# Kernel optimization log

Hardware: AMD Instinct MI355X
Metric: run time of the kernel (lower is better)

Reference implementation:

```python
import jax, jax.numpy as jnp
import numpy as np

B, S, D_IN, D_OUT = 4, 4096, 1024, 1024

def setup_inputs() -> dict:
    key = jax.random.key(0)
    kx, kq, kk, kv = jax.random.split(key, 4)
    # torch Linear weights are [out, in]; init scale ~ U(-1/sqrt(in), 1/sqrt(in))
    lim = 1.0 / np.sqrt(D_IN)
    x = jax.random.normal(kx, (B, S, D_IN), dtype=jnp.float32)
    W_query = jax.random.uniform(kq, (D_OUT, D_IN), dtype=jnp.float32, minval=-lim, maxval=lim)
    W_key = jax.random.uniform(kk, (D_OUT, D_IN), dtype=jnp.float32, minval=-lim, maxval=lim)
    W_value = jax.random.uniform(kv, (D_OUT, D_IN), dtype=jnp.float32, minval=-lim, maxval=lim)
    return {"x": x, "W_query": W_query, "W_key": W_key, "W_value": W_value}

def reference(x, W_query, W_key, W_value):
    # Linear: x @ W.T  (torch convention, weight shape [out, in])
    q = jnp.einsum('bsd,od->bso', x, W_query)
    k = jnp.einsum('bsd,od->bso', x, W_key)
    v = jnp.einsum('bsd,od->bso', x, W_value)
    scale = 1.0 / jnp.sqrt(jnp.asarray(k.shape[-1], dtype=x.dtype))
    scores = jnp.einsum('bqo,bko->bqk', q, k) * scale  # [B,S,S]
    weights = jax.nn.softmax(scores, axis=-1)
    return jnp.einsum('bqk,bko->bqo', weights, v)  # [B,S,D_OUT]
```

## Files before the change

### kernel.cpp

```cpp
#include <hip/hip_runtime.h>
#include <cstdint>
#include <cstddef>

typedef __attribute__((ext_vector_type(8))) short short8;
typedef __attribute__((ext_vector_type(4))) float f32x4;

__device__ __forceinline__ unsigned short f2bf(float x) {
  union { float f; unsigned u; } v; v.f = x;
  unsigned r = (v.u + 0x7FFFu + ((v.u >> 16) & 1u)) >> 16;
  return (unsigned short)r;
}

#define GLOAD16(g, l)                                                    \
  __builtin_amdgcn_global_load_lds(                                      \
      (const __attribute__((address_space(1))) unsigned int*)(g),        \
      (__attribute__((address_space(3))) unsigned int*)(l), 16, 0, 0)

__global__ __launch_bounds__(256) void cvt_f32_bf16(
    const float* __restrict__ in, unsigned short* __restrict__ out, long n) {
  long i = ((long)blockIdx.x * 256 + threadIdx.x) * 8;
  if (i >= n) return;
  const float4* p = (const float4*)(in + i);
  float4 a = p[0], b = p[1];
  short8 r;
  r[0] = (short)f2bf(a.x); r[1] = (short)f2bf(a.y);
  r[2] = (short)f2bf(a.z); r[3] = (short)f2bf(a.w);
  r[4] = (short)f2bf(b.x); r[5] = (short)f2bf(b.y);
  r[6] = (short)f2bf(b.z); r[7] = (short)f2bf(b.w);
  *(short8*)(out + i) = r;
}

template <int MODE>
__global__ __launch_bounds__(512, 2) void gemm_bt256(
    const unsigned short* __restrict__ A, int lda, size_t asb,
    const unsigned short* __restrict__ B, int ldb, size_t bsb,
    void* __restrict__ C, int ldc, size_t csb,
    int nbn, int K, float scale) {
  __shared__ unsigned short As[2][256 * 64];
  __shared__ unsigned short Bs[2][256 * 64];

  A += (size_t)blockIdx.y * asb;
  B += (size_t)blockIdx.y * bsb;
  char* Cb = (char*)C + (size_t)blockIdx.y * csb * (MODE == 3 ? 4 : 2);

  unsigned bid = blockIdx.x;
  unsigned cpx = gridDim.x >> 3;
  unsigned swz = (bid & 7u) * cpx + (bid >> 3);
  int bm = (int)(swz / (unsigned)nbn);
  int bn = (int)(swz % (unsigned)nbn);
  int m0 = bm * 256, n0 = bn * 256;

  int t512 = threadIdx.x;
  int lane = t512 & 63, wid = t512 >> 6;
  int wm = wid >> 2, wn = wid & 3;
  int l15 = lane & 15, l4 = lane >> 4;

  int srow = t512 >> 3;
  int g = (t512 & 7) ^ ((t512 >> 3) & 7);
  const unsigned short* pa = A + (size_t)(m0 + srow) * lda + g * 8;
  const unsigned short* pb = B + (size_t)(n0 + srow) * ldb + g * 8;

  f32x4 acc[8][4] = {};
  f32x4 rsum[8] = {};
  short8 ones;
#pragma unroll
  for (int e = 0; e < 8; e++) ones[e] = (short)0x3F80;

  const int NT = K >> 6;

#define STAGE(jj, buf)                                                    \
  do {                                                                    \
    int _k0 = (jj) << 6;                                                  \
    _Pragma("unroll") for (int i = 0; i < 4; i++)                         \
        GLOAD16(pa + (size_t)(i * 64) * lda + _k0,                        \
                (char*)As[buf] + i * 8192 + t512 * 16);                   \
    _Pragma("unroll") for (int i = 0; i < 4; i++)                         \
        GLOAD16(pb + (size_t)(i * 64) * ldb + _k0,                        \
                (char*)Bs[buf] + i * 8192 + t512 * 16);                   \
  } while (0)

  STAGE(0, 0);

  for (int j = 0; j < NT; ++j) {
    int cur = j & 1;
    __builtin_amdgcn_sched_barrier(0);
    __builtin_amdgcn_s_barrier();
    if (j + 1 < NT) {
      STAGE(j + 1, cur ^ 1);
      asm volatile("s_waitcnt vmcnt(8)" ::: "memory");
    } else {
      asm volatile("s_waitcnt vmcnt(0)" ::: "memory");
    }
    __builtin_amdgcn_s_barrier();

    const char* Ab = (const char*)As[cur];
    const char* Bb = (const char*)Bs[cur];

    short8 bfv[4][2], afv[8][2];
#pragma unroll
    for (int ni = 0; ni < 4; ni++)
#pragma unroll
      for (int ks = 0; ks < 2; ks++) {
        int r = wn * 64 + ni * 16 + l15;
        int c = ((ks << 2) | l4) ^ (r & 7);
        bfv[ni][ks] = *(const short8*)(Bb + r * 128 + c * 16);
      }
#pragma unroll
    for (int mi = 0; mi < 8; mi++)
#pragma unroll
      for (int ks = 0; ks < 2; ks++) {
        int r = wm * 128 + mi * 16 + l15;
        int c = ((ks << 2) | l4) ^ (r & 7);
        afv[mi][ks] = *(const short8*)(Ab + r * 128 + c * 16);
      }
#pragma unroll
    for (int ks = 0; ks < 2; ks++)
#pragma unroll
      for (int mi = 0; mi < 8; mi++) {
#pragma unroll
        for (int ni = 0; ni < 4; ni++)
          acc[mi][ni] = __builtin_amdgcn_mfma_f32_16x16x32_bf16(
              afv[mi][ks], bfv[ni][ks], acc[mi][ni], 0, 0, 0);
        if constexpr (MODE == 3)
          rsum[mi] = __builtin_amdgcn_mfma_f32_16x16x32_bf16(
              afv[mi][ks], ones, rsum[mi], 0, 0, 0);
      }
  }
#undef STAGE

#pragma unroll
  for (int mi = 0; mi < 8; mi++) {
    float inv[4];
    if constexpr (MODE == 3) {
#pragma unroll
      for (int jj = 0; jj < 4; jj++) inv[jj] = 1.0f / rsum[mi][jj];
    }
#pragma unroll
    for (int ni = 0; ni < 4; ni++)
#pragma unroll
      for (int jj = 0; jj < 4; jj++) {
        int row = m0 + wm * 128 + mi * 16 + l4 * 4 + jj;
        int col = n0 + wn * 64 + ni * 16 + l15;
        float val = acc[mi][ni][jj];
        if constexpr (MODE == 1) {
          ((unsigned short*)Cb)[(size_t)row * ldc + col] = f2bf(val * scale);
        } else if constexpr (MODE == 2) {
          ((unsigned short*)Cb)[(size_t)row * ldc + col] =
              f2bf(__expf(val * scale));
        } else {
          ((float*)Cb)[(size_t)row * ldc + col] = val * inv[jj];
        }
      }
  }
}

extern "C" void kernel_launch(void* const* d_in, const int* in_sizes, int n_in,
                              void* d_out, int out_size, void* d_ws, size_t ws_size,
                              hipStream_t stream) {
  (void)in_sizes; (void)n_in; (void)out_size;
  const float* x  = (const float*)d_in[0];
  const float* Wq = (const float*)d_in[1];
  const float* Wk = (const float*)d_in[2];
  const float* Wv = (const float*)d_in[3];
  float* out = (float*)d_out;

  const int Bn = 4, S = 4096, D = 1024;
  const size_t MS = (size_t)Bn * S;
  const float scale = 0.03125f;

  char* ws = (char*)d_ws;
  unsigned short* QKb = (unsigned short*)ws; ws += MS * 2048 * 2;
  unsigned short* VTb = (unsigned short*)ws; ws += MS * D * 2;
  unsigned short* Sreg = (unsigned short*)ws;
  const size_t s4_bytes = (size_t)Bn * S * S * 2;
  const size_t s1_bytes = (size_t)S * S * 2;
  size_t head = (size_t)(ws - (char*)d_ws);
  bool batched = ws_size >= head + s4_bytes + 6u * 1024 * 1024;
  ws += batched ? s4_bytes : s1_bytes;
  unsigned short* wqkb = (unsigned short*)ws; ws += (size_t)2048 * D * 2;
  unsigned short* wvb  = (unsigned short*)ws;
  unsigned short* xb = Sreg;

  cvt_f32_bf16<<<8192, 256, 0, stream>>>(x, xb, (long)MS * D);
  cvt_f32_bf16<<<512, 256, 0, stream>>>(Wq, wqkb, (long)D * D);
  cvt_f32_bf16<<<512, 256, 0, stream>>>(Wk, wqkb + (size_t)D * D, (long)D * D);
  cvt_f32_bf16<<<512, 256, 0, stream>>>(Wv, wvb, (long)D * D);

  gemm_bt256<1><<<dim3(512, 1), 512, 0, stream>>>(
      xb, D, 0, wqkb, D, 0, QKb, 2048, 0, 8, D, 1.0f);
  gemm_bt256<1><<<dim3(256, 1), 512, 0, stream>>>(
      wvb, D, 0, xb, D, 0, VTb, (int)MS, 0, 64, D, 1.0f);

  if (batched) {
    gemm_bt256<2><<<dim3(256, Bn), 512, 0, stream>>>(
        QKb, 2048, (size_t)S * 2048,
        QKb + 1024, 2048, (size_t)S * 2048,
        Sreg, S, (size_t)S * S, 16, D, scale);
    gemm_bt256<3><<<dim3(64, Bn), 512, 0, stream>>>(
        Sreg, S, (size_t)S * S,
        VTb, (int)MS, (size_t)S,
        out, D, (size_t)S * D, 4, S, 1.0f);
  } else {
    for (int b = 0; b < Bn; b++) {
      const unsigned short* Qx = QKb + (size_t)b * S * 2048;
      const unsigned short* Kx = Qx + 1024;
      gemm_bt256<2><<<dim3(256, 1), 512, 0, stream>>>(
          Qx, 2048, 0, Kx, 2048, 0, Sreg, S, 0, 16, D, scale);
      gemm_bt256<3><<<dim3(64, 1), 512, 0, stream>>>(
          Sreg, S, 0, VTb + (size_t)b * S, (int)MS, 0,
          out + (size_t)b * S * D, D, 0, 4, S, 1.0f);
    }
  }
}
```

Measured before the change: 455.4 us.

## Shrink GEMM tiles to 256x128x32 and move softmax row sums into score epilogue

Reworks the shared GEMM kernel to use 256x128 output tiles with a K-step of 32, smaller LDS buffers and a new swizzle, with launch bounds raised to 4 blocks per CU for higher occupancy. The softmax denominator is no longer computed by extra MFMAs against a ones vector in the PV GEMM. Instead the exp epilogue of the score GEMM reduces row sums with shuffles and atomically adds them into a memset workspace buffer. It also brackets the MFMA loop with setprio. The cost is more blocks, less data reuse per tile, fp32 atomics and an extra memset, and the row sums now come from unrounded fp32 exp values instead of the bf16-stored ones.

```diff
diff --git a/kernel.cpp b/kernel.cpp
--- a/kernel.cpp
+++ b/kernel.cpp
@@ -31,52 +31,48 @@
 }
 
 template <int MODE>
-__global__ __launch_bounds__(512, 2) void gemm_bt256(
+__global__ __launch_bounds__(512, 4) void gemm_bt(
     const unsigned short* __restrict__ A, int lda, size_t asb,
     const unsigned short* __restrict__ B, int ldb, size_t bsb,
     void* __restrict__ C, int ldc, size_t csb,
+    float* __restrict__ rs, int rss,
     int nbn, int K, float scale) {
-  __shared__ unsigned short As[2][256 * 64];
-  __shared__ unsigned short Bs[2][256 * 64];
+  __shared__ unsigned short As[2][256 * 32];
+  __shared__ unsigned short Bs[2][128 * 32];
 
   A += (size_t)blockIdx.y * asb;
   B += (size_t)blockIdx.y * bsb;
   char* Cb = (char*)C + (size_t)blockIdx.y * csb * (MODE == 3 ? 4 : 2);
+  rs += (size_t)blockIdx.y * rss;
 
   unsigned bid = blockIdx.x;
   unsigned cpx = gridDim.x >> 3;
   unsigned swz = (bid & 7u) * cpx + (bid >> 3);
   int bm = (int)(swz / (unsigned)nbn);
   int bn = (int)(swz % (unsigned)nbn);
-  int m0 = bm * 256, n0 = bn * 256;
+  int m0 = bm * 256, n0 = bn * 128;
 
   int t512 = threadIdx.x;
   int lane = t512 & 63, wid = t512 >> 6;
-  int wm = wid >> 2, wn = wid & 3;
+  int wm = wid >> 1, wn = wid & 1;
   int l15 = lane & 15, l4 = lane >> 4;
 
-  int srow = t512 >> 3;
-  int g = (t512 & 7) ^ ((t512 >> 3) & 7);
+  int srow = t512 >> 2;
+  int g = (t512 & 3) ^ ((t512 >> 3) & 3);
   const unsigned short* pa = A + (size_t)(m0 + srow) * lda + g * 8;
   const unsigned short* pb = B + (size_t)(n0 + srow) * ldb + g * 8;
 
-  f32x4 acc[8][4] = {};
-  f32x4 rsum[8] = {};
-  short8 ones;
-#pragma unroll
-  for (int e = 0; e < 8; e++) ones[e] = (short)0x3F80;
-
-  const int NT = K >> 6;
-
-#define STAGE(jj, buf)                                                    \
-  do {                                                                    \
-    int _k0 = (jj) << 6;                                                  \
-    _Pragma("unroll") for (int i = 0; i < 4; i++)                         \
-        GLOAD16(pa + (size_t)(i * 64) * lda + _k0,                        \
-                (char*)As[buf] + i * 8192 + t512 * 16);                   \
-    _Pragma("unroll") for (int i = 0; i < 4; i++)                         \
-        GLOAD16(pb + (size_t)(i * 64) * ldb + _k0,                        \
-                (char*)Bs[buf] + i * 8192 + t512 * 16);                   \
+  f32x4 acc[4][4] = {};
+
+  const int NT = K >> 5;
+
+#define STAGE(jj, buf)                                                   \
+  do {                                                                   \
+    int _k0 = (jj) << 5;                                                 \
+    GLOAD16(pa + _k0, (char*)As[buf] + t512 * 16);                       \
+    GLOAD16(pa + (size_t)128 * lda + _k0,                                \
+            (char*)As[buf] + 8192 + t512 * 16);                          \
+    GLOAD16(pb + _k0, (char*)Bs[buf] + t512 * 16);                       \
   } while (0)
 
   STAGE(0, 0);
@@ -87,7 +83,7 @@
     __builtin_amdgcn_s_barrier();
     if (j + 1 < NT) {
       STAGE(j + 1, cur ^ 1);
-      asm volatile("s_waitcnt vmcnt(8)" ::: "memory");
+      asm volatile("s_waitcnt vmcnt(3)" ::: "memory");
     } else {
       asm volatile("s_waitcnt vmcnt(0)" ::: "memory");
     }
@@ -96,61 +92,86 @@
     const char* Ab = (const char*)As[cur];
     const char* Bb = (const char*)Bs[cur];
 
-    short8 bfv[4][2], afv[8][2];
-#pragma unroll
-    for (int ni = 0; ni < 4; ni++)
-#pragma unroll
-      for (int ks = 0; ks < 2; ks++) {
-        int r = wn * 64 + ni * 16 + l15;
-        int c = ((ks << 2) | l4) ^ (r & 7);
-        bfv[ni][ks] = *(const short8*)(Bb + r * 128 + c * 16);
-      }
-#pragma unroll
-    for (int mi = 0; mi < 8; mi++)
-#pragma unroll
-      for (int ks = 0; ks < 2; ks++) {
-        int r = wm * 128 + mi * 16 + l15;
-        int c = ((ks << 2) | l4) ^ (r & 7);
-        afv[mi][ks] = *(const short8*)(Ab + r * 128 + c * 16);
-      }
-#pragma unroll
-    for (int ks = 0; ks < 2; ks++)
-#pragma unroll
-      for (int mi = 0; mi < 8; mi++) {
-#pragma unroll
-        for (int ni = 0; ni < 4; ni++)
-          acc[mi][ni] = __builtin_amdgcn_mfma_f32_16x16x32_bf16(
-              afv[mi][ks], bfv[ni][ks], acc[mi][ni], 0, 0, 0);
-        if constexpr (MODE == 3)
-          rsum[mi] = __builtin_amdgcn_mfma_f32_16x16x32_bf16(
-              afv[mi][ks], ones, rsum[mi], 0, 0, 0);
-      }
+    short8 bfv[4], afv[4];
+#pragma unroll
+    for (int ni = 0; ni < 4; ni++) {
+      int r = wn * 64 + ni * 16 + l15;
+      int slot = l4 ^ ((r >> 1) & 3);
+      bfv[ni] = *(const short8*)(Bb + r * 64 + slot * 16);
+    }
+#pragma unroll
+    for (int mi = 0; mi < 4; mi++) {
+      int r = wm * 64 + mi * 16 + l15;
+      int slot = l4 ^ ((r >> 1) & 3);
+      afv[mi] = *(const short8*)(Ab + r * 64 + slot * 16);
+    }
+    __builtin_amdgcn_s_setprio(1);
+#pragma unroll
+    for (int mi = 0; mi < 4; mi++)
+#pragma unroll
+      for (int ni = 0; ni < 4; ni++)
+        acc[mi][ni] = __builtin_amdgcn_mfma_f32_16x16x32_bf16(
+            afv[mi], bfv[ni], acc[mi][ni], 0, 0, 0);
+    __builtin_amdgcn_s_setprio(0);
   }
 #undef STAGE
 
-#pragma unroll
-  for (int mi = 0; mi < 8; mi++) {
-    float inv[4];
-    if constexpr (MODE == 3) {
-#pragma unroll
-      for (int jj = 0; jj < 4; jj++) inv[jj] = 1.0f / rsum[mi][jj];
-    }
-#pragma unroll
-    for (int ni = 0; ni < 4; ni++)
+  if constexpr (MODE == 2) {
+    float sums[4][4];
+#pragma unroll
+    for (int mi = 0; mi < 4; mi++)
+#pragma unroll
+      for (int jj = 0; jj < 4; jj++) sums[mi][jj] = 0.f;
+#pragma unroll
+    for (int mi = 0; mi < 4; mi++)
+#pragma unroll
+      for (int ni = 0; ni < 4; ni++)
+#pragma unroll
+        for (int jj = 0; jj < 4; jj++) {
+          int row = m0 + wm * 64 + mi * 16 + l4 * 4 + jj;
+          int col = n0 + wn * 64 + ni * 16 + l15;
+          float e = __expf(acc[mi][ni][jj] * scale);
+          sums[mi][jj] += e;
+          ((unsigned short*)Cb)[(size_t)row * ldc + col] = f2bf(e);
+        }
+#pragma unroll
+    for (int mi = 0; mi < 4; mi++)
 #pragma unroll
       for (int jj = 0; jj < 4; jj++) {
-        int row = m0 + wm * 128 + mi * 16 + l4 * 4 + jj;
-        int col = n0 + wn * 64 + ni * 16 + l15;
-        float val = acc[mi][ni][jj];
-        if constexpr (MODE == 1) {
-          ((unsigned short*)Cb)[(size_t)row * ldc + col] = f2bf(val * scale);
-        } else if constexpr (MODE == 2) {
-          ((unsigned short*)Cb)[(size_t)row * ldc + col] =
-              f2bf(__expf(val * scale));
-        } else {
-          ((float*)Cb)[(size_t)row * ldc + col] = val * inv[jj];
+        float s = sums[mi][jj];
+        s += __shfl_xor(s, 1);
+        s += __shfl_xor(s, 2);
+        s += __shfl_xor(s, 4);
+        s += __shfl_xor(s, 8);
+        if (l15 == 0) {
+          int row = m0 + wm * 64 + mi * 16 + l4 * 4 + jj;
+          atomicAdd(&rs[row], s);
         }
       }
+  } else {
+#pragma unroll
+    for (int mi = 0; mi < 4; mi++) {
+      float inv[4];
+      if constexpr (MODE == 3) {
+#pragma unroll
+        for (int jj = 0; jj < 4; jj++) {
+          int row = m0 + wm * 64 + mi * 16 + l4 * 4 + jj;
+          inv[jj] = 1.0f / rs[row];
+        }
+      }
+#pragma unroll
+      for (int ni = 0; ni < 4; ni++)
+#pragma unroll
+        for (int jj = 0; jj < 4; jj++) {
+          int row = m0 + wm * 64 + mi * 16 + l4 * 4 + jj;
+          int col = n0 + wn * 64 + ni * 16 + l15;
+          float val = acc[mi][ni][jj];
+          if constexpr (MODE == 1)
+            ((unsigned short*)Cb)[(size_t)row * ldc + col] = f2bf(val * scale);
+          else
+            ((float*)Cb)[(size_t)row * ldc + col] = val * inv[jj];
+        }
+    }
   }
 }
 
@@ -175,40 +196,44 @@
   const size_t s4_bytes = (size_t)Bn * S * S * 2;
   const size_t s1_bytes = (size_t)S * S * 2;
   size_t head = (size_t)(ws - (char*)d_ws);
-  bool batched = ws_size >= head + s4_bytes + 6u * 1024 * 1024;
+  bool batched = ws_size >= head + s4_bytes + 8u * 1024 * 1024;
   ws += batched ? s4_bytes : s1_bytes;
   unsigned short* wqkb = (unsigned short*)ws; ws += (size_t)2048 * D * 2;
-  unsigned short* wvb  = (unsigned short*)ws;
+  unsigned short* wvb  = (unsigned short*)ws; ws += (size_t)D * D * 2;
+  float* rsum = (float*)ws;
   unsigned short* xb = Sreg;
+
+  hipMemsetAsync(rsum, 0, MS * sizeof(float), stream);
 
   cvt_f32_bf16<<<8192, 256, 0, stream>>>(x, xb, (long)MS * D);
   cvt_f32_bf16<<<512, 256, 0, stream>>>(Wq, wqkb, (long)D * D);
   cvt_f32_bf16<<<512, 256, 0, stream>>>(Wk, wqkb + (size_t)D * D, (long)D * D);
   cvt_f32_bf16<<<512, 256, 0, stream>>>(Wv, wvb, (long)D * D);
 
-  gemm_bt256<1><<<dim3(512, 1), 512, 0, stream>>>(
-      xb, D, 0, wqkb, D, 0, QKb, 2048, 0, 8, D, 1.0f);
-  gemm_bt256<1><<<dim3(256, 1), 512, 0, stream>>>(
-      wvb, D, 0, xb, D, 0, VTb, (int)MS, 0, 64, D, 1.0f);
+  gemm_bt<1><<<dim3(1024, 1), 512, 0, stream>>>(
+      xb, D, 0, wqkb, D, 0, QKb, 2048, 0, nullptr, 0, 16, D, 1.0f);
+  gemm_bt<1><<<dim3(512, 1), 512, 0, stream>>>(
+      wvb, D, 0, xb, D, 0, VTb, (int)MS, 0, nullptr, 0, 128, D, 1.0f);
 
   if (batched) {
-    gemm_bt256<2><<<dim3(256, Bn), 512, 0, stream>>>(
+    gemm_bt<2><<<dim3(512, Bn), 512, 0, stream>>>(
         QKb, 2048, (size_t)S * 2048,
         QKb + 1024, 2048, (size_t)S * 2048,
-        Sreg, S, (size_t)S * S, 16, D, scale);
-    gemm_bt256<3><<<dim3(64, Bn), 512, 0, stream>>>(
+        Sreg, S, (size_t)S * S, rsum, S, 32, D, scale);
+    gemm_bt<3><<<dim3(128, Bn), 512, 0, stream>>>(
         Sreg, S, (size_t)S * S,
         VTb, (int)MS, (size_t)S,
-        out, D, (size_t)S * D, 4, S, 1.0f);
+        out, D, (size_t)S * D, rsum, S, 8, S, 1.0f);
   } else {
     for (int b = 0; b < Bn; b++) {
       const unsigned short* Qx = QKb + (size_t)b * S * 2048;
       const unsigned short* Kx = Qx + 1024;
-      gemm_bt256<2><<<dim3(256, 1), 512, 0, stream>>>(
-          Qx, 2048, 0, Kx, 2048, 0, Sreg, S, 0, 16, D, scale);
-      gemm_bt256<3><<<dim3(64, 1), 512, 0, stream>>>(
+      gemm_bt<2><<<dim3(512, 1), 512, 0, stream>>>(
+          Qx, 2048, 0, Kx, 2048, 0, Sreg, S, 0, rsum + (size_t)b * S, 0,
+          32, D, scale);
+      gemm_bt<3><<<dim3(128, 1), 512, 0, stream>>>(
           Sreg, S, 0, VTb + (size_t)b * S, (int)MS, 0,
-          out + (size_t)b * S * D, D, 0, 4, S, 1.0f);
+          out + (size_t)b * S * D, D, 0, rsum + (size_t)b * S, 0, 8, S, 1.0f);
     }
   }
 }
```

New measurement: 465.1 us. 2.1% more time.
